# Performance work log

Hardware: AMD Instinct MI355X
Metric: run time of the kernel (lower is better)

The kernel has to match this reference:

```python
import jax, jax.numpy as jnp
import numpy as np


def _roi_bilinear(image, roi, pool):
    """Crop image[y:y+h, x:x+w] and bilinearly resize to (pool, pool).

    Matches tf.image.resize bilinear (half-pixel centers, no antialias) on the
    dynamically-cropped region, but expressed as a fused gather+interpolate on
    the full image so it is jit-able with static shapes.
    image: [H, W, C] float; roi: [4] int32 = (x, y, w, h).
    """
    x, y, w, h = roi[0], roi[1], roi[2], roi[3]

    def axis_coords(offset, size):
        size_f = size.astype(jnp.float32)
        scale = size_f / pool
        src = (jnp.arange(pool, dtype=jnp.float32) + 0.5) * scale - 0.5
        src = jnp.clip(src, 0.0, size_f - 1.0)
        i0 = jnp.floor(src).astype(jnp.int32)
        i1 = jnp.minimum(i0 + 1, size - 1)
        frac = src - i0.astype(jnp.float32)
        return offset + i0, offset + i1, frac

    y0, y1, fy = axis_coords(y, h)  # [pool]
    x0, x1, fx = axis_coords(x, w)  # [pool]

    v00 = image[y0[:, None], x0[None, :], :]  # [pool, pool, C]
    v01 = image[y0[:, None], x1[None, :], :]
    v10 = image[y1[:, None], x0[None, :], :]
    v11 = image[y1[:, None], x1[None, :], :]

    fy = fy[:, None, None]
    fx = fx[None, :, None]
    top = v00 * (1.0 - fx) + v01 * fx
    bot = v10 * (1.0 - fx) + v11 * fx
    return top * (1.0 - fy) + bot * fy


def setup_inputs() -> dict:
    key = jax.random.key(0)
    k_img, k_xy, k_wh = jax.random.split(key, 3)
    H = W = 128
    C = 512
    num_rois = 256
    image = jax.random.normal(k_img, (1, H, W, C), dtype=jnp.float32)
    xy = jax.random.randint(k_xy, (1, num_rois, 2), 0, 64, dtype=jnp.int32)
    wh = jax.random.randint(k_wh, (1, num_rois, 2), 1, 64, dtype=jnp.int32)
    rois = jnp.concatenate([xy, wh], axis=-1)  # [1, num_rois, 4] = (x, y, w, h)
    return {"image": image, "rois": rois, "pool_size": 14}


def reference(image, rois, pool_size):
    # image: [1, H, W, C]; rois: [1, num_rois, 4] int32 (x, y, w, h)
    img = image[0]
    out = jax.vmap(lambda r: _roi_bilinear(img, r, pool_size))(rois[0])
    # [1, num_rois, pool, pool, C]
    return out[None]
```

## Files before the change

### kernel.cpp

```cpp
#include <hip/hip_runtime.h>
#include <hip/hip_bf16.h>


__global__ __launch_bounds__(128)
void roi_bilinear_kernel(const float* __restrict__ img,
                         const int*   __restrict__ rois,
                         float*       __restrict__ out,
                         int W, int C, int pool) {
    const int pix = blockIdx.x;
    const int px  = pix % pool;
    const int tmp = pix / pool;
    const int py  = tmp % pool;
    const int roi = tmp / pool;

    const int4 rv = reinterpret_cast<const int4*>(rois)[roi];
    const float poolf = (float)pool;

    const float hf = (float)rv.w;
    float sy = ((float)py + 0.5f) * (hf / poolf) - 0.5f;
    sy = fminf(fmaxf(sy, 0.0f), hf - 1.0f);
    const int   i0y = (int)floorf(sy);
    const int   i1y = min(i0y + 1, rv.w - 1);
    const float fy  = sy - (float)i0y;
    const int   y0  = rv.y + i0y;
    const int   y1  = rv.y + i1y;

    const float wf = (float)rv.z;
    float sx = ((float)px + 0.5f) * (wf / poolf) - 0.5f;
    sx = fminf(fmaxf(sx, 0.0f), wf - 1.0f);
    const int   i0x = (int)floorf(sx);
    const int   i1x = min(i0x + 1, rv.z - 1);
    const float fx  = sx - (float)i0x;
    const int   x0  = rv.x + i0x;
    const int   x1  = rv.x + i1x;

    const int C4 = C >> 2;
    const int c4 = threadIdx.x;

    const float4* imgv = reinterpret_cast<const float4*>(img);
    const size_t b00 = (size_t)(y0 * W + x0) * C4 + c4;
    const size_t b01 = (size_t)(y0 * W + x1) * C4 + c4;
    const size_t b10 = (size_t)(y1 * W + x0) * C4 + c4;
    const size_t b11 = (size_t)(y1 * W + x1) * C4 + c4;

    const float4 v00 = imgv[b00];
    const float4 v01 = imgv[b01];
    const float4 v10 = imgv[b10];
    const float4 v11 = imgv[b11];

    const float gx = 1.0f - fx;
    const float gy = 1.0f - fy;

    float4 o;
    o.x = (v00.x * gx + v01.x * fx) * gy + (v10.x * gx + v11.x * fx) * fy;
    o.y = (v00.y * gx + v01.y * fx) * gy + (v10.y * gx + v11.y * fx) * fy;
    o.z = (v00.z * gx + v01.z * fx) * gy + (v10.z * gx + v11.z * fx) * fy;
    o.w = (v00.w * gx + v01.w * fx) * gy + (v10.w * gx + v11.w * fx) * fy;

    reinterpret_cast<float4*>(out)[(size_t)pix * C4 + c4] = o;
}

extern "C" void kernel_launch(void* const* d_in, const int* in_sizes, int n_in,
                              void* d_out, int out_size, void* d_ws, size_t ws_size,
                              hipStream_t stream) {
    const float* img  = (const float*)d_in[0];
    const int*   rois = (const int*)d_in[1];
    float* out = (float*)d_out;

    const int H = 128, W = 128, C = 512;
    (void)H;
    const int num_rois = in_sizes[1] / 4;

    const int pp = out_size / (num_rois * C);
    int pool = 1;
    while ((pool + 1) * (pool + 1) <= pp) ++pool;

    const int npix = num_rois * pool * pool;
    const int C4 = C / 4;
    roi_bilinear_kernel<<<npix, C4, 0, stream>>>(img, rois, out, W, C, pool);
}
```

Before: 158.8 us.

## Process one ROI output row per block with XCD-aware block remapping

Each block now handles a whole output row (roi, py) using 256 threads, two pixels at a time over the x loop, in place of one pixel per 128-thread block. Block IDs are remapped so consecutive rows of the same ROI land on the same XCD, which should improve L2 reuse of the shared image rows. Output stores become nontemporal to avoid polluting cache with write-only data. This cuts launch and per-block overhead and reuses the y-coordinate setup. The trade-off is less parallelism per block and a loop with an odd trip count when pool is odd.

```diff
diff --git a/kernel.cpp b/kernel.cpp
--- a/kernel.cpp
+++ b/kernel.cpp
@@ -2,16 +2,27 @@
 #include <hip/hip_bf16.h>
 
 
-__global__ __launch_bounds__(128)
-void roi_bilinear_kernel(const float* __restrict__ img,
-                         const int*   __restrict__ rois,
-                         float*       __restrict__ out,
-                         int W, int C, int pool) {
-    const int pix = blockIdx.x;
-    const int px  = pix % pool;
-    const int tmp = pix / pool;
-    const int py  = tmp % pool;
-    const int roi = tmp / pool;
+typedef float vfloat4 __attribute__((ext_vector_type(4)));
+
+__global__ __launch_bounds__(256)
+void roi_bilinear_row_kernel(const float* __restrict__ img,
+                             const int*   __restrict__ rois,
+                             float*       __restrict__ out,
+                             int W, int pool, int nroi) {
+    const int C4 = 128;
+    const int nblk = nroi * pool;
+
+    int lin;
+    if ((nblk & 7) == 0) {
+        const int per_xcd = nblk >> 3;
+        const int xcd = blockIdx.x & 7;
+        const int j   = blockIdx.x >> 3;
+        lin = xcd * per_xcd + j;
+    } else {
+        lin = blockIdx.x;
+    }
+    const int roi = lin / pool;
+    const int py  = lin - roi * pool;
 
     const int4 rv = reinterpret_cast<const int4*>(rois)[roi];
     const float poolf = (float)pool;
@@ -24,40 +35,42 @@
     const float fy  = sy - (float)i0y;
     const int   y0  = rv.y + i0y;
     const int   y1  = rv.y + i1y;
+    const float gy  = 1.0f - fy;
 
     const float wf = (float)rv.z;
-    float sx = ((float)px + 0.5f) * (wf / poolf) - 0.5f;
-    sx = fminf(fmaxf(sx, 0.0f), wf - 1.0f);
-    const int   i0x = (int)floorf(sx);
-    const int   i1x = min(i0x + 1, rv.z - 1);
-    const float fx  = sx - (float)i0x;
-    const int   x0  = rv.x + i0x;
-    const int   x1  = rv.x + i1x;
+    const float xscale = wf / poolf;
+    const float xmax = wf - 1.0f;
+    const int   xlim = rv.z - 1;
 
-    const int C4 = C >> 2;
-    const int c4 = threadIdx.x;
+    const int c4  = threadIdx.x & (C4 - 1);
+    const int sub = threadIdx.x >> 7;
 
-    const float4* imgv = reinterpret_cast<const float4*>(img);
-    const size_t b00 = (size_t)(y0 * W + x0) * C4 + c4;
-    const size_t b01 = (size_t)(y0 * W + x1) * C4 + c4;
-    const size_t b10 = (size_t)(y1 * W + x0) * C4 + c4;
-    const size_t b11 = (size_t)(y1 * W + x1) * C4 + c4;
+    const vfloat4* __restrict__ imgv = reinterpret_cast<const vfloat4*>(img);
+    vfloat4* __restrict__ outv = reinterpret_cast<vfloat4*>(out);
 
-    const float4 v00 = imgv[b00];
-    const float4 v01 = imgv[b01];
-    const float4 v10 = imgv[b10];
-    const float4 v11 = imgv[b11];
+    const size_t row0 = (size_t)(y0 * W) * C4 + c4;
+    const size_t row1 = (size_t)(y1 * W) * C4 + c4;
+    const size_t outbase = (size_t)lin * pool * C4 + c4;
 
-    const float gx = 1.0f - fx;
-    const float gy = 1.0f - fy;
+    for (int px = sub; px < pool; px += 2) {
+        float sx = ((float)px + 0.5f) * xscale - 0.5f;
+        sx = fminf(fmaxf(sx, 0.0f), xmax);
+        const int   i0x = (int)floorf(sx);
+        const int   i1x = min(i0x + 1, xlim);
+        const float fx  = sx - (float)i0x;
+        const int   x0  = (rv.x + i0x) * C4;
+        const int   x1  = (rv.x + i1x) * C4;
 
-    float4 o;
-    o.x = (v00.x * gx + v01.x * fx) * gy + (v10.x * gx + v11.x * fx) * fy;
-    o.y = (v00.y * gx + v01.y * fx) * gy + (v10.y * gx + v11.y * fx) * fy;
-    o.z = (v00.z * gx + v01.z * fx) * gy + (v10.z * gx + v11.z * fx) * fy;
-    o.w = (v00.w * gx + v01.w * fx) * gy + (v10.w * gx + v11.w * fx) * fy;
+        const vfloat4 v00 = imgv[row0 + x0];
+        const vfloat4 v01 = imgv[row0 + x1];
+        const vfloat4 v10 = imgv[row1 + x0];
+        const vfloat4 v11 = imgv[row1 + x1];
 
-    reinterpret_cast<float4*>(out)[(size_t)pix * C4 + c4] = o;
+        const float gx = 1.0f - fx;
+        vfloat4 o = (v00 * gx + v01 * fx) * gy + (v10 * gx + v11 * fx) * fy;
+
+        __builtin_nontemporal_store(o, &outv[outbase + (size_t)px * C4]);
+    }
 }
 
 extern "C" void kernel_launch(void* const* d_in, const int* in_sizes, int n_in,
@@ -67,15 +80,14 @@
     const int*   rois = (const int*)d_in[1];
     float* out = (float*)d_out;
 
-    const int H = 128, W = 128, C = 512;
-    (void)H;
+    const int W = 128, C = 512;
     const int num_rois = in_sizes[1] / 4;
 
     const int pp = out_size / (num_rois * C);
     int pool = 1;
     while ((pool + 1) * (pool + 1) <= pp) ++pool;
 
-    const int npix = num_rois * pool * pool;
-    const int C4 = C / 4;
-    roi_bilinear_kernel<<<npix, C4, 0, stream>>>(img, rois, out, W, C, pool);
+    const int nblk = num_rois * pool;
+    roi_bilinear_row_kernel<<<nblk, 256, 0, stream>>>(img, rois, out,
+                                                      W, pool, num_rois);
 }
```

New measurement: 156.4 us (median of 2 runs). Within noise of the previous version (-1.5%).
